# Performance work log

Hardware: AMD Instinct MI355X
Metric: run time of the kernel (lower is better)

Reference implementation:

```python
import jax, jax.numpy as jnp
import numpy as np

N_NODES = 50000
N_EDGES = 800000
IN_DIM = 256
EMB_DIM = 128


def setup_inputs() -> dict:
    key = jax.random.key(0)
    ks = jax.random.split(key, 12)
    x = jax.random.normal(ks[0], (N_NODES, IN_DIM), dtype=jnp.float32)
    edge_index = jax.random.randint(ks[1], (2, N_EDGES), 0, N_NODES, dtype=jnp.int32)
    # Layer 1 params (GCNConv in=256 out=128 with bias, LayerNorm gamma/beta)
    W1 = jax.random.normal(ks[2], (IN_DIM, EMB_DIM), dtype=jnp.float32) / np.sqrt(IN_DIM)
    b1 = jnp.zeros((EMB_DIM,), jnp.float32)
    g1 = jnp.ones((EMB_DIM,), jnp.float32)
    be1 = jnp.zeros((EMB_DIM,), jnp.float32)
    # Layer 2 params (GCNConv in=128 out=128, LayerNorm)
    W2 = jax.random.normal(ks[3], (EMB_DIM, EMB_DIM), dtype=jnp.float32) / np.sqrt(EMB_DIM)
    b2 = jnp.zeros((EMB_DIM,), jnp.float32)
    g2 = jnp.ones((EMB_DIM,), jnp.float32)
    be2 = jnp.zeros((EMB_DIM,), jnp.float32)
    return {"x": x, "W1": W1, "b1": b1, "g1": g1, "be1": be1,
            "W2": W2, "b2": b2, "g2": g2, "be2": be2,
            "edge_index": edge_index}


def _gcn_conv(x, W, b, src, dst, n_nodes):
    # PyG GCNConv: h = x @ W; add self-loops; sym-normalize; scatter-add to dst; + bias
    h = x @ W                                   # [N, out]
    loop = jnp.arange(n_nodes, dtype=src.dtype)
    src_f = jnp.concatenate([src, loop])        # [E+N]
    dst_f = jnp.concatenate([dst, loop])
    deg = jax.ops.segment_sum(jnp.ones_like(dst_f, dtype=h.dtype), dst_f,
                              num_segments=n_nodes)
    dinv = jnp.where(deg > 0, jax.lax.rsqrt(deg), 0.0)
    norm = dinv[src_f] * dinv[dst_f]            # [E+N]
    msg = h[src_f] * norm[:, None]              # gather + scale (memory-bound)
    out = jax.ops.segment_sum(msg, dst_f, num_segments=n_nodes)
    return out + b


def _layer_norm(x, gamma, beta, eps=1e-5):
    mu = jnp.mean(x, axis=-1, keepdims=True)
    var = jnp.mean(jnp.square(x - mu), axis=-1, keepdims=True)
    return (x - mu) * jax.lax.rsqrt(var + eps) * gamma + beta


def reference(x, W1, b1, g1, be1, W2, b2, g2, be2, edge_index):
    src, dst = edge_index[0], edge_index[1]
    n = x.shape[0]
    # Layer 1: in_dim (256) != embed_dim (128) -> no residual
    h = _gcn_conv(x, W1, b1, src, dst, n)
    h = jax.nn.elu(_layer_norm(h, g1, be1))      # dropout = identity (eval mode)
    # Layer 2: dims match -> residual
    res = h
    h2 = _gcn_conv(h, W2, b2, src, dst, n)
    h2 = jax.nn.elu(_layer_norm(h2, g2, be2))
    return h2 + res
```

## Files before the change

kernel.cpp:

```cpp
#include <hip/hip_runtime.h>
#include <hip/hip_bf16.h>

#define NN 50000
#define NE 800000
#define KDIM 256
#define EMB 128
#define NB 391
#define CAP 2560
#define HB 196
#define CWB 192
#define NG1 196
#define NG2 391

typedef unsigned short u16;
typedef __attribute__((ext_vector_type(8))) short short8;
typedef __attribute__((ext_vector_type(4))) float f32x4;

static __device__ __forceinline__ u16 f2bf(float f) {
    union { float f; unsigned int u; } x; x.f = f;
    unsigned int u = x.u;
    unsigned int r = (u + 0x7fffu + ((u >> 16) & 1u)) >> 16;
    return (u16)r;
}
static __device__ __forceinline__ float bf2f(u16 b) {
    union { unsigned int u; float f; } x; x.u = ((unsigned int)b) << 16;
    return x.f;
}
static __device__ __forceinline__ unsigned cvtpk(float lo, float hi) {
    unsigned r;
    asm volatile("v_cvt_pk_bf16_f32 %0, %1, %2" : "=v"(r) : "v"(lo), "v"(hi));
    return r;
}

__global__ __launch_bounds__(256) void prep_kernel(const float* __restrict__ W1,
                                                   const float* __restrict__ W2,
                                                   u16* __restrict__ Wt1,
                                                   u16* __restrict__ Wt2,
                                                   int* __restrict__ bcnt) {
    if (blockIdx.x == CWB) {
        int t = threadIdx.x;
        if (t < NB) bcnt[t] = 0;
        if (t + 256 < NB) bcnt[t + 256] = 0;
        return;
    }
    int i = blockIdx.x * 256 + threadIdx.x;
    if (i < 128 * 256) {
        int n = i >> 8, k = i & 255;
        Wt1[i] = f2bf(W1[k * 128 + n]);
    } else {
        int j = i - 128 * 256;
        if (j < 128 * 128) {
            int n = j >> 7, k = j & 127;
            Wt2[j] = f2bf(W2[k * 128 + n]);
        }
    }
}

template <int K, bool A_BF16, bool FUSE_PA>
__global__ __launch_bounds__(512) void gemm_kernel(
    const void* __restrict__ Av, const u16* __restrict__ Bt, u16* __restrict__ C, int M,
    const int* __restrict__ esrc, const int* __restrict__ edst,
    int* __restrict__ bcnt, unsigned int* __restrict__ packed, int E) {
    __shared__ u16 Bs[128 * K];

    if constexpr (FUSE_PA) {
        if (blockIdx.x < HB) {
            int* hist = (int*)Bs;
            int* base = hist + NB;
            int t = threadIdx.x;
            int i0 = blockIdx.x * 4096;
            int i1 = i0 + 4096 < E ? i0 + 4096 : E;
            for (int b = t; b < NB; b += 512) hist[b] = 0;
            __syncthreads();
            for (int i = i0 + t; i < i1; i += 512) atomicAdd(&hist[edst[i] >> 7], 1);
            __syncthreads();
            for (int b = t; b < NB; b += 512) {
                int c = hist[b];
                base[b] = c ? atomicAdd(&bcnt[b], c) : 0;
                hist[b] = 0;
            }
            __syncthreads();
            for (int i = i0 + t; i < i1; i += 512) {
                int d = edst[i];
                int b = d >> 7;
                int off = base[b] + atomicAdd(&hist[b], 1);
                if (off < CAP)
                    packed[b * CAP + off] = ((unsigned int)esrc[i] << 7) | (unsigned int)(d & 127);
            }
            return;
        }
    }

    int gb = FUSE_PA ? (blockIdx.x - HB) : blockIdx.x;
    int ngb = FUSE_PA ? (gridDim.x - HB) : gridDim.x;
    int tid = threadIdx.x;
    int wave = tid >> 6, lane = tid & 63;
    constexpr int NKS = K / 32;
    constexpr int NCH = 128 * K / 8;
#pragma unroll
    for (int i = 0; i < NCH / 512; i++) {
        int idx = tid + i * 512;
        int n = idx / (K / 8), c = idx % (K / 8);
        int k0 = c * 8;
        uint4 v = *(const uint4*)(Bt + (size_t)n * K + k0);
        *(uint4*)&Bs[(((n >> 4) * NKS + (k0 >> 5)) << 9) + ((n & 15) << 5) + (k0 & 31)] = v;
    }
    __syncthreads();

    int arow = lane & 15;
    int kb = (lane >> 4) * 8;
    int nfrag = (M + 15) / 16;
    for (int frag = gb * 8 + wave; frag < nfrag; frag += ngb * 8) {
        int row0 = frag * 16;
        short8 af[NKS];
        int r = row0 + arow;
        if (r > M - 1) r = M - 1;
        if constexpr (!A_BF16) {
            const float* ap = (const float*)Av + (size_t)r * K + kb;
#pragma unroll
            for (int ks = 0; ks < NKS; ks++) {
                float4 v0 = *(const float4*)(ap + ks * 32);
                float4 v1 = *(const float4*)(ap + ks * 32 + 4);
                uint4 u;
                u.x = cvtpk(v0.x, v0.y);
                u.y = cvtpk(v0.z, v0.w);
                u.z = cvtpk(v1.x, v1.y);
                u.w = cvtpk(v1.z, v1.w);
                af[ks] = *(short8*)&u;
            }
        } else {
            const u16* ap = (const u16*)Av + (size_t)r * K + kb;
#pragma unroll
            for (int ks = 0; ks < NKS; ks++) {
                uint4 u = *(const uint4*)(ap + ks * 32);
                af[ks] = *(short8*)&u;
            }
        }
        f32x4 acc[8];
#pragma unroll
        for (int nf = 0; nf < 8; nf++) acc[nf] = (f32x4){0.f, 0.f, 0.f, 0.f};
#pragma unroll
        for (int ks = 0; ks < NKS; ks++) {
#pragma unroll
            for (int nf = 0; nf < 8; nf++) {
                short8 b = *(const short8*)&Bs[((nf * NKS + ks) << 9) + (arow << 5) + kb];
                acc[nf] = __builtin_amdgcn_mfma_f32_16x16x32_bf16(af[ks], b, acc[nf], 0, 0, 0);
            }
        }
        int rb = row0 + (lane >> 4) * 4;
        int col = lane & 15;
#pragma unroll
        for (int nf = 0; nf < 8; nf++)
#pragma unroll
            for (int rr = 0; rr < 4; rr++) {
                int grow = rb + rr;
                if (grow < M) C[(size_t)grow * 128 + nf * 16 + col] = f2bf(acc[nf][rr]);
            }
    }
}

__global__ __launch_bounds__(256) void passB_kernel(const unsigned int* __restrict__ packed,
                                                    const int* __restrict__ bcnt,
                                                    u16* __restrict__ srcs,
                                                    unsigned int* __restrict__ rowinfo,
                                                    float* __restrict__ dinv, int n) {
    __shared__ int lc[128];
    __shared__ int cur[128];
    int b = blockIdx.x, t = threadIdx.x;
    int nb0 = b << 7;
    int nnodes = (n - nb0) < 128 ? (n - nb0) : 128;
    int cnt = bcnt[b];
    if (cnt > CAP) cnt = CAP;
    int e0 = b * CAP;
    int e1 = e0 + cnt;
    if (t < 128) lc[t] = 0;
    __syncthreads();
    for (int i = e0 + t; i < e1; i += 256) atomicAdd(&lc[packed[i] & 127], 1);
    __syncthreads();
    int myc = (t < 128) ? lc[t] : 0;
    for (int off = 1; off < 128; off <<= 1) {
        int a = (t < 128 && t >= off) ? lc[t - off] : 0;
        __syncthreads();
        if (t < 128) lc[t] += a;
        __syncthreads();
    }
    if (t < 128) {
        int excl = e0 + lc[t] - myc;
        cur[t] = excl;
        if (t < nnodes) {
            rowinfo[nb0 + t] = ((unsigned int)excl << 12) | (unsigned int)myc;
            dinv[nb0 + t] = rsqrtf((float)(myc + 1));
        }
    }
    __syncthreads();
    for (int i = e0 + t; i < e1; i += 256) {
        unsigned int v = packed[i];
        int p = atomicAdd(&cur[v & 127], 1);
        srcs[p] = (u16)(v >> 7);
    }
}

template <bool HAS_RES, bool OUT_BF16>
__global__ __launch_bounds__(256) void agg_kernel(
    const u16* __restrict__ h, const unsigned int* __restrict__ rowinfo,
    const u16* __restrict__ srcs, const float* __restrict__ dinv,
    const float* __restrict__ bias, const float* __restrict__ gamma,
    const float* __restrict__ beta, const u16* __restrict__ resid,
    void* __restrict__ outv, int n) {
    int wave = threadIdx.x >> 6, lane = threadIdx.x & 63;
    int node = blockIdx.x * 4 + wave;
    if (node >= n) return;
    unsigned int ri = rowinfo[node];
    int e0 = ri >> 12;
    int e1 = e0 + (ri & 4095);
    float di = dinv[node];
    int half = lane >> 5, sl = lane & 31;
    float a0 = 0.f, a1 = 0.f, a2 = 0.f, a3 = 0.f;
    for (int base = e0; base < e1; base += 64) {
        int nE = e1 - base;
        if (nE > 64) nE = 64;
        int s = (lane < nE) ? (int)srcs[base + lane] : 0;
        float w = ((lane < nE) ? dinv[s] : 0.f) * di;
        for (int jp = 0; jp < nE; jp += 4) {
            int i0 = jp + half;
            int i1 = jp + 2 + half;
            int ss0 = __shfl(s, i0); float w0 = __shfl(w, i0);
            int ss1 = __shfl(s, i1); float w1 = __shfl(w, i1);
            uint2 v0 = *(const uint2*)(h + (size_t)ss0 * 128 + sl * 4);
            uint2 v1 = *(const uint2*)(h + (size_t)ss1 * 128 + sl * 4);
            a0 += bf2f((u16)v0.x) * w0 + bf2f((u16)v1.x) * w1;
            a1 += bf2f((u16)(v0.x >> 16)) * w0 + bf2f((u16)(v1.x >> 16)) * w1;
            a2 += bf2f((u16)v0.y) * w0 + bf2f((u16)v1.y) * w1;
            a3 += bf2f((u16)(v0.y >> 16)) * w0 + bf2f((u16)(v1.y >> 16)) * w1;
        }
    }
    {
        uint2 v = *(const uint2*)(h + (size_t)node * 128 + sl * 4);
        float sw = (half == 0) ? di * di : 0.f;
        a0 += bf2f((u16)v.x) * sw;
        a1 += bf2f((u16)(v.x >> 16)) * sw;
        a2 += bf2f((u16)v.y) * sw;
        a3 += bf2f((u16)(v.y >> 16)) * sw;
    }
    a0 += __shfl_xor(a0, 32);
    a1 += __shfl_xor(a1, 32);
    a2 += __shfl_xor(a2, 32);
    a3 += __shfl_xor(a3, 32);
    a0 += bias[sl * 4];
    a1 += bias[sl * 4 + 1];
    a2 += bias[sl * 4 + 2];
    a3 += bias[sl * 4 + 3];
    float sum = a0 + a1 + a2 + a3;
    float sq = a0 * a0 + a1 * a1 + a2 * a2 + a3 * a3;
    for (int off = 16; off >= 1; off >>= 1) {
        sum += __shfl_xor(sum, off);
        sq += __shfl_xor(sq, off);
    }
    float mu = sum * (1.f / 128.f);
    float var = sq * (1.f / 128.f) - mu * mu;
    float rs = rsqrtf(var + 1e-5f);
    float o0 = (a0 - mu) * rs * gamma[sl * 4] + beta[sl * 4];
    float o1 = (a1 - mu) * rs * gamma[sl * 4 + 1] + beta[sl * 4 + 1];
    float o2 = (a2 - mu) * rs * gamma[sl * 4 + 2] + beta[sl * 4 + 2];
    float o3 = (a3 - mu) * rs * gamma[sl * 4 + 3] + beta[sl * 4 + 3];
    o0 = o0 > 0.f ? o0 : __expf(o0) - 1.f;
    o1 = o1 > 0.f ? o1 : __expf(o1) - 1.f;
    o2 = o2 > 0.f ? o2 : __expf(o2) - 1.f;
    o3 = o3 > 0.f ? o3 : __expf(o3) - 1.f;
    if constexpr (HAS_RES) {
        uint2 rv = *(const uint2*)(resid + (size_t)node * 128 + sl * 4);
        o0 += bf2f((u16)rv.x);
        o1 += bf2f((u16)(rv.x >> 16));
        o2 += bf2f((u16)rv.y);
        o3 += bf2f((u16)(rv.y >> 16));
    }
    if (half == 0) {
        if constexpr (OUT_BF16) {
            u16* out = (u16*)outv;
            uint2 pk;
            pk.x = (unsigned)f2bf(o0) | ((unsigned)f2bf(o1) << 16);
            pk.y = (unsigned)f2bf(o2) | ((unsigned)f2bf(o3) << 16);
            *(uint2*)(out + (size_t)node * 128 + sl * 4) = pk;
        } else {
            float* out = (float*)outv;
            *(float4*)(out + (size_t)node * 128 + sl * 4) = make_float4(o0, o1, o2, o3);
        }
    }
}

extern "C" void kernel_launch(void* const* d_in, const int* in_sizes, int n_in,
                              void* d_out, int out_size, void* d_ws, size_t ws_size,
                              hipStream_t stream) {
    const float* x   = (const float*)d_in[0];
    const float* W1  = (const float*)d_in[1];
    const float* b1  = (const float*)d_in[2];
    const float* g1  = (const float*)d_in[3];
    const float* be1 = (const float*)d_in[4];
    const float* W2  = (const float*)d_in[5];
    const float* b2  = (const float*)d_in[6];
    const float* g2  = (const float*)d_in[7];
    const float* be2 = (const float*)d_in[8];
    const int* ei    = (const int*)d_in[9];
    const int* srcp  = ei;
    const int* dstp  = ei + NE;
    float* out = (float*)d_out;

    char* ws = (char*)d_ws;
    size_t off = 0;
    auto alloc = [&](size_t bytes) {
        void* p = ws + off;
        off += (bytes + 255) & ~(size_t)255;
        return p;
    };
    int* bcnt        = (int*)alloc(NB * 4);
    unsigned* rowinfo= (unsigned*)alloc(NN * 4);
    float* dinv      = (float*)alloc(NN * 4);
    unsigned* packed = (unsigned*)alloc((size_t)NB * CAP * 4);
    u16* srcs_s      = (u16*)alloc((size_t)NB * CAP * 2);
    u16* Wt1         = (u16*)alloc(128 * 256 * 2);
    u16* Wt2         = (u16*)alloc(128 * 128 * 2);
    u16* hb          = (u16*)alloc((size_t)NN * 128 * 2);
    u16* h1b         = (u16*)alloc((size_t)NN * 128 * 2);

    prep_kernel<<<CWB + 1, 256, 0, stream>>>(W1, W2, Wt1, Wt2, bcnt);
    gemm_kernel<256, false, true><<<HB + NG1, 512, 0, stream>>>(x, Wt1, hb, NN,
                                                                srcp, dstp, bcnt, packed, NE);
    passB_kernel<<<NB, 256, 0, stream>>>(packed, bcnt, srcs_s, rowinfo, dinv, NN);
    agg_kernel<false, true><<<(NN + 3) / 4, 256, 0, stream>>>(hb, rowinfo, srcs_s, dinv,
                                                              b1, g1, be1, nullptr, h1b, NN);
    gemm_kernel<128, true, false><<<NG2, 512, 0, stream>>>(h1b, Wt2, hb, NN,
                                                           nullptr, nullptr, nullptr, nullptr, 0);
    agg_kernel<true, false><<<(NN + 3) / 4, 256, 0, stream>>>(hb, rowinfo, srcs_s, dinv,
                                                              b2, g2, be2, h1b, out, NN);
}
```

Baseline: 129.8 us.

## Split aggregation into feature-sliced gather and separate LayerNorm pass with permuted layout

Splits each aggregation into two kernels. The first gathers neighbour rows one 16-feature slice at a time, with eight blocks per 128-node bucket each owning one slice, so the gathered slice of h is reused from cache. The second applies bias, LayerNorm, ELU and the residual. The GEMM epilogue now writes packed 16-byte stores in a permuted column order. Parameters, W2 rows and the final fp32 output are remapped to match that order. This adds an extra bf16 round-trip through a new hagg buffer, a rounding step before LayerNorm, and scattered fp32 output stores.

```diff
diff --git a/kernel.cpp b/kernel.cpp
--- a/kernel.cpp
+++ b/kernel.cpp
@@ -13,6 +13,7 @@
 #define NG2 391
 
 typedef unsigned short u16;
+typedef unsigned char u8;
 typedef __attribute__((ext_vector_type(8))) short short8;
 typedef __attribute__((ext_vector_type(4))) float f32x4;
 
@@ -31,16 +32,27 @@
     asm volatile("v_cvt_pk_bf16_f32 %0, %1, %2" : "=v"(r) : "v"(lo), "v"(hi));
     return r;
 }
-
-__global__ __launch_bounds__(256) void prep_kernel(const float* __restrict__ W1,
-                                                   const float* __restrict__ W2,
-                                                   u16* __restrict__ Wt1,
-                                                   u16* __restrict__ Wt2,
-                                                   int* __restrict__ bcnt) {
+static __device__ __forceinline__ int p2dim(int p) { return ((p & 7) << 4) + (p >> 3); }
+
+__global__ __launch_bounds__(256) void prep_kernel(
+    const float* __restrict__ W1, const float* __restrict__ W2,
+    u16* __restrict__ Wt1, u16* __restrict__ Wt2, int* __restrict__ bcnt,
+    const float* __restrict__ b1, const float* __restrict__ g1, const float* __restrict__ be1,
+    const float* __restrict__ b2, const float* __restrict__ g2, const float* __restrict__ be2,
+    float* __restrict__ prm) {
     if (blockIdx.x == CWB) {
         int t = threadIdx.x;
         if (t < NB) bcnt[t] = 0;
         if (t + 256 < NB) bcnt[t + 256] = 0;
+        if (t < 128) {
+            int d = p2dim(t);
+            prm[t]       = b1[d];
+            prm[128 + t] = g1[d];
+            prm[256 + t] = be1[d];
+            prm[384 + t] = b2[d];
+            prm[512 + t] = g2[d];
+            prm[640 + t] = be2[d];
+        }
         return;
     }
     int i = blockIdx.x * 256 + threadIdx.x;
@@ -50,15 +62,16 @@
     } else {
         int j = i - 128 * 256;
         if (j < 128 * 128) {
-            int n = j >> 7, k = j & 127;
-            Wt2[j] = f2bf(W2[k * 128 + n]);
+            int n = j >> 7, p = j & 127;
+            Wt2[j] = f2bf(W2[p2dim(p) * 128 + n]);
         }
     }
 }
 
 template <int K, bool A_BF16, bool FUSE_PA>
 __global__ __launch_bounds__(512) void gemm_kernel(
-    const void* __restrict__ Av, const u16* __restrict__ Bt, u16* __restrict__ C, int M,
+    const void* __restrict__ Av, const u16* __restrict__ Bt,
+    u16* __restrict__ Cb, int M,
     const int* __restrict__ esrc, const int* __restrict__ edst,
     int* __restrict__ bcnt, unsigned int* __restrict__ packed, int E) {
     __shared__ u16 Bs[128 * K];
@@ -150,12 +163,17 @@
         int rb = row0 + (lane >> 4) * 4;
         int col = lane & 15;
 #pragma unroll
-        for (int nf = 0; nf < 8; nf++)
-#pragma unroll
-            for (int rr = 0; rr < 4; rr++) {
-                int grow = rb + rr;
-                if (grow < M) C[(size_t)grow * 128 + nf * 16 + col] = f2bf(acc[nf][rr]);
-            }
+        for (int rr = 0; rr < 4; rr++) {
+            int grow = rb + rr;
+            if (grow < M) {
+                uint4 pb;
+                pb.x = cvtpk(acc[0][rr], acc[1][rr]);
+                pb.y = cvtpk(acc[2][rr], acc[3][rr]);
+                pb.z = cvtpk(acc[4][rr], acc[5][rr]);
+                pb.w = cvtpk(acc[6][rr], acc[7][rr]);
+                *(uint4*)(Cb + (size_t)grow * 128 + col * 8) = pb;
+            }
+        }
     }
 }
 
@@ -200,91 +218,84 @@
     }
 }
 
-template <bool HAS_RES, bool OUT_BF16>
-__global__ __launch_bounds__(256) void agg_kernel(
+__global__ __launch_bounds__(256) void aggA_kernel(
     const u16* __restrict__ h, const unsigned int* __restrict__ rowinfo,
     const u16* __restrict__ srcs, const float* __restrict__ dinv,
-    const float* __restrict__ bias, const float* __restrict__ gamma,
-    const float* __restrict__ beta, const u16* __restrict__ resid,
-    void* __restrict__ outv, int n) {
+    u16* __restrict__ hagg, int n) {
+    int dg = blockIdx.x & 7;
+    int bucket = blockIdx.x >> 3;
+    int wave = threadIdx.x >> 6, lane = threadIdx.x & 63;
+    int slot = lane >> 3, j = lane & 7;
+    int doff = dg * 16 + j * 2;
+    int n0 = bucket * 128 + wave * 32;
+    for (int ni = 0; ni < 32; ni++) {
+        int node = n0 + ni;
+        if (node >= n) break;
+        unsigned ri = rowinfo[node];
+        int e0 = ri >> 12;
+        int cnt = ri & 4095;
+        float di = dinv[node];
+        float a0 = 0.f, a1 = 0.f;
+        for (int jp = 0; jp < cnt; jp += 8) {
+            int idx = jp + slot;
+            int valid = idx < cnt;
+            int s = valid ? (int)srcs[e0 + idx] : 0;
+            float w = valid ? dinv[s] * di : 0.f;
+            unsigned v = *(const unsigned*)(h + (size_t)s * 128 + doff);
+            a0 += bf2f((u16)v) * w;
+            a1 += bf2f((u16)(v >> 16)) * w;
+        }
+        {
+            unsigned v = *(const unsigned*)(h + (size_t)node * 128 + doff);
+            float sw = (slot == 0) ? di * di : 0.f;
+            a0 += bf2f((u16)v) * sw;
+            a1 += bf2f((u16)(v >> 16)) * sw;
+        }
+        a0 += __shfl_xor(a0, 8);  a1 += __shfl_xor(a1, 8);
+        a0 += __shfl_xor(a0, 16); a1 += __shfl_xor(a1, 16);
+        a0 += __shfl_xor(a0, 32); a1 += __shfl_xor(a1, 32);
+        if (slot == 0)
+            *(unsigned*)(hagg + (size_t)node * 128 + doff) = cvtpk(a0, a1);
+    }
+}
+
+template <bool HAS_RES, bool OUT_BF16>
+__global__ __launch_bounds__(256) void aggB_kernel(
+    const u16* __restrict__ hagg, const float* __restrict__ prm, int prmoff,
+    const u16* __restrict__ resid, void* __restrict__ outv, int n) {
     int wave = threadIdx.x >> 6, lane = threadIdx.x & 63;
     int node = blockIdx.x * 4 + wave;
     if (node >= n) return;
-    unsigned int ri = rowinfo[node];
-    int e0 = ri >> 12;
-    int e1 = e0 + (ri & 4095);
-    float di = dinv[node];
-    int half = lane >> 5, sl = lane & 31;
-    float a0 = 0.f, a1 = 0.f, a2 = 0.f, a3 = 0.f;
-    for (int base = e0; base < e1; base += 64) {
-        int nE = e1 - base;
-        if (nE > 64) nE = 64;
-        int s = (lane < nE) ? (int)srcs[base + lane] : 0;
-        float w = ((lane < nE) ? dinv[s] : 0.f) * di;
-        for (int jp = 0; jp < nE; jp += 4) {
-            int i0 = jp + half;
-            int i1 = jp + 2 + half;
-            int ss0 = __shfl(s, i0); float w0 = __shfl(w, i0);
-            int ss1 = __shfl(s, i1); float w1 = __shfl(w, i1);
-            uint2 v0 = *(const uint2*)(h + (size_t)ss0 * 128 + sl * 4);
-            uint2 v1 = *(const uint2*)(h + (size_t)ss1 * 128 + sl * 4);
-            a0 += bf2f((u16)v0.x) * w0 + bf2f((u16)v1.x) * w1;
-            a1 += bf2f((u16)(v0.x >> 16)) * w0 + bf2f((u16)(v1.x >> 16)) * w1;
-            a2 += bf2f((u16)v0.y) * w0 + bf2f((u16)v1.y) * w1;
-            a3 += bf2f((u16)(v0.y >> 16)) * w0 + bf2f((u16)(v1.y >> 16)) * w1;
-        }
-    }
-    {
-        uint2 v = *(const uint2*)(h + (size_t)node * 128 + sl * 4);
-        float sw = (half == 0) ? di * di : 0.f;
-        a0 += bf2f((u16)v.x) * sw;
-        a1 += bf2f((u16)(v.x >> 16)) * sw;
-        a2 += bf2f((u16)v.y) * sw;
-        a3 += bf2f((u16)(v.y >> 16)) * sw;
-    }
-    a0 += __shfl_xor(a0, 32);
-    a1 += __shfl_xor(a1, 32);
-    a2 += __shfl_xor(a2, 32);
-    a3 += __shfl_xor(a3, 32);
-    a0 += bias[sl * 4];
-    a1 += bias[sl * 4 + 1];
-    a2 += bias[sl * 4 + 2];
-    a3 += bias[sl * 4 + 3];
-    float sum = a0 + a1 + a2 + a3;
-    float sq = a0 * a0 + a1 * a1 + a2 * a2 + a3 * a3;
-    for (int off = 16; off >= 1; off >>= 1) {
+    const float* bias = prm + prmoff;
+    const float* gamma = bias + 128;
+    const float* beta = gamma + 128;
+    unsigned v = *(const unsigned*)(hagg + (size_t)node * 128 + lane * 2);
+    float a0 = bf2f((u16)v) + bias[lane * 2];
+    float a1 = bf2f((u16)(v >> 16)) + bias[lane * 2 + 1];
+    float sum = a0 + a1, sq = a0 * a0 + a1 * a1;
+    for (int off = 32; off >= 1; off >>= 1) {
         sum += __shfl_xor(sum, off);
         sq += __shfl_xor(sq, off);
     }
     float mu = sum * (1.f / 128.f);
     float var = sq * (1.f / 128.f) - mu * mu;
     float rs = rsqrtf(var + 1e-5f);
-    float o0 = (a0 - mu) * rs * gamma[sl * 4] + beta[sl * 4];
-    float o1 = (a1 - mu) * rs * gamma[sl * 4 + 1] + beta[sl * 4 + 1];
-    float o2 = (a2 - mu) * rs * gamma[sl * 4 + 2] + beta[sl * 4 + 2];
-    float o3 = (a3 - mu) * rs * gamma[sl * 4 + 3] + beta[sl * 4 + 3];
+    float o0 = (a0 - mu) * rs * gamma[lane * 2] + beta[lane * 2];
+    float o1 = (a1 - mu) * rs * gamma[lane * 2 + 1] + beta[lane * 2 + 1];
     o0 = o0 > 0.f ? o0 : __expf(o0) - 1.f;
     o1 = o1 > 0.f ? o1 : __expf(o1) - 1.f;
-    o2 = o2 > 0.f ? o2 : __expf(o2) - 1.f;
-    o3 = o3 > 0.f ? o3 : __expf(o3) - 1.f;
     if constexpr (HAS_RES) {
-        uint2 rv = *(const uint2*)(resid + (size_t)node * 128 + sl * 4);
-        o0 += bf2f((u16)rv.x);
-        o1 += bf2f((u16)(rv.x >> 16));
-        o2 += bf2f((u16)rv.y);
-        o3 += bf2f((u16)(rv.y >> 16));
-    }
-    if (half == 0) {
-        if constexpr (OUT_BF16) {
-            u16* out = (u16*)outv;
-            uint2 pk;
-            pk.x = (unsigned)f2bf(o0) | ((unsigned)f2bf(o1) << 16);
-            pk.y = (unsigned)f2bf(o2) | ((unsigned)f2bf(o3) << 16);
-            *(uint2*)(out + (size_t)node * 128 + sl * 4) = pk;
-        } else {
-            float* out = (float*)outv;
-            *(float4*)(out + (size_t)node * 128 + sl * 4) = make_float4(o0, o1, o2, o3);
-        }
+        unsigned rv = *(const unsigned*)(resid + (size_t)node * 128 + lane * 2);
+        o0 += bf2f((u16)rv);
+        o1 += bf2f((u16)(rv >> 16));
+    }
+    if constexpr (OUT_BF16) {
+        *(unsigned*)((u16*)outv + (size_t)node * 128 + lane * 2) = cvtpk(o0, o1);
+    } else {
+        float* out = (float*)outv + (size_t)node * 128;
+        int p = lane * 2;
+        out[p2dim(p)] = o0;
+        out[p2dim(p + 1)] = o1;
     }
 }
 
@@ -315,21 +326,24 @@
     int* bcnt        = (int*)alloc(NB * 4);
     unsigned* rowinfo= (unsigned*)alloc(NN * 4);
     float* dinv      = (float*)alloc(NN * 4);
+    float* prm       = (float*)alloc(6 * 128 * 4);
     unsigned* packed = (unsigned*)alloc((size_t)NB * CAP * 4);
     u16* srcs_s      = (u16*)alloc((size_t)NB * CAP * 2);
     u16* Wt1         = (u16*)alloc(128 * 256 * 2);
     u16* Wt2         = (u16*)alloc(128 * 128 * 2);
     u16* hb          = (u16*)alloc((size_t)NN * 128 * 2);
+    u16* hagg        = (u16*)alloc((size_t)NN * 128 * 2);
     u16* h1b         = (u16*)alloc((size_t)NN * 128 * 2);
 
-    prep_kernel<<<CWB + 1, 256, 0, stream>>>(W1, W2, Wt1, Wt2, bcnt);
+    prep_kernel<<<CWB + 1, 256, 0, stream>>>(W1, W2, Wt1, Wt2, bcnt,
+                                             b1, g1, be1, b2, g2, be2, prm);
     gemm_kernel<256, false, true><<<HB + NG1, 512, 0, stream>>>(x, Wt1, hb, NN,
                                                                 srcp, dstp, bcnt, packed, NE);
     passB_kernel<<<NB, 256, 0, stream>>>(packed, bcnt, srcs_s, rowinfo, dinv, NN);
-    agg_kernel<false, true><<<(NN + 3) / 4, 256, 0, stream>>>(hb, rowinfo, srcs_s, dinv,
-                                                              b1, g1, be1, nullptr, h1b, NN);
+    aggA_kernel<<<NB * 8, 256, 0, stream>>>(hb, rowinfo, srcs_s, dinv, hagg, NN);
+    aggB_kernel<false, true><<<(NN + 3) / 4, 256, 0, stream>>>(hagg, prm, 0, nullptr, h1b, NN);
     gemm_kernel<128, true, false><<<NG2, 512, 0, stream>>>(h1b, Wt2, hb, NN,
                                                            nullptr, nullptr, nullptr, nullptr, 0);
-    agg_kernel<true, false><<<(NN + 3) / 4, 256, 0, stream>>>(hb, rowinfo, srcs_s, dinv,
-                                                              b2, g2, be2, h1b, out, NN);
-}
+    aggA_kernel<<<NB * 8, 256, 0, stream>>>(hb, rowinfo, srcs_s, dinv, hagg, NN);
+    aggB_kernel<true, false><<<(NN + 3) / 4, 256, 0, stream>>>(hagg, prm, 384, h1b, out, NN);
+}
```

Measured after the change: 456.4 us. +251.5%, slower.

## Store GEMM output in permuted column order with packed 16-byte row writes

Applied to the files above, without the earlier changes.

The GEMM epilogue now packs the eight accumulator fragments per row into one 16-byte bf16 store, replacing scattered 2-byte stores. The hidden dimension is therefore kept in a permuted order. W2 rows, bias, gamma and beta are pre-permuted to match, and the final fp32 output is un-permuted with scalar stores. The layer-1 GEMM grid size also changes. The cost is scattered 4-byte final output writes in place of float4 stores.

```diff
diff --git a/kernel.cpp b/kernel.cpp
--- a/kernel.cpp
+++ b/kernel.cpp
@@ -9,10 +9,11 @@
 #define CAP 2560
 #define HB 196
 #define CWB 192
-#define NG1 196
+#define NG1 316
 #define NG2 391
 
 typedef unsigned short u16;
+typedef unsigned char u8;
 typedef __attribute__((ext_vector_type(8))) short short8;
 typedef __attribute__((ext_vector_type(4))) float f32x4;
 
@@ -31,16 +32,27 @@
     asm volatile("v_cvt_pk_bf16_f32 %0, %1, %2" : "=v"(r) : "v"(lo), "v"(hi));
     return r;
 }
-
-__global__ __launch_bounds__(256) void prep_kernel(const float* __restrict__ W1,
-                                                   const float* __restrict__ W2,
-                                                   u16* __restrict__ Wt1,
-                                                   u16* __restrict__ Wt2,
-                                                   int* __restrict__ bcnt) {
+static __device__ __forceinline__ int p2dim(int p) { return ((p & 7) << 4) + (p >> 3); }
+
+__global__ __launch_bounds__(256) void prep_kernel(
+    const float* __restrict__ W1, const float* __restrict__ W2,
+    u16* __restrict__ Wt1, u16* __restrict__ Wt2, int* __restrict__ bcnt,
+    const float* __restrict__ b1, const float* __restrict__ g1, const float* __restrict__ be1,
+    const float* __restrict__ b2, const float* __restrict__ g2, const float* __restrict__ be2,
+    float* __restrict__ prm) {
     if (blockIdx.x == CWB) {
         int t = threadIdx.x;
         if (t < NB) bcnt[t] = 0;
         if (t + 256 < NB) bcnt[t + 256] = 0;
+        if (t < 128) {
+            int d = p2dim(t);
+            prm[t]       = b1[d];
+            prm[128 + t] = g1[d];
+            prm[256 + t] = be1[d];
+            prm[384 + t] = b2[d];
+            prm[512 + t] = g2[d];
+            prm[640 + t] = be2[d];
+        }
         return;
     }
     int i = blockIdx.x * 256 + threadIdx.x;
@@ -50,15 +62,16 @@
     } else {
         int j = i - 128 * 256;
         if (j < 128 * 128) {
-            int n = j >> 7, k = j & 127;
-            Wt2[j] = f2bf(W2[k * 128 + n]);
+            int n = j >> 7, p = j & 127;
+            Wt2[j] = f2bf(W2[p2dim(p) * 128 + n]);
         }
     }
 }
 
 template <int K, bool A_BF16, bool FUSE_PA>
 __global__ __launch_bounds__(512) void gemm_kernel(
-    const void* __restrict__ Av, const u16* __restrict__ Bt, u16* __restrict__ C, int M,
+    const void* __restrict__ Av, const u16* __restrict__ Bt,
+    u16* __restrict__ Cb, int M,
     const int* __restrict__ esrc, const int* __restrict__ edst,
     int* __restrict__ bcnt, unsigned int* __restrict__ packed, int E) {
     __shared__ u16 Bs[128 * K];
@@ -150,12 +163,17 @@
         int rb = row0 + (lane >> 4) * 4;
         int col = lane & 15;
 #pragma unroll
-        for (int nf = 0; nf < 8; nf++)
-#pragma unroll
-            for (int rr = 0; rr < 4; rr++) {
-                int grow = rb + rr;
-                if (grow < M) C[(size_t)grow * 128 + nf * 16 + col] = f2bf(acc[nf][rr]);
-            }
+        for (int rr = 0; rr < 4; rr++) {
+            int grow = rb + rr;
+            if (grow < M) {
+                uint4 pb;
+                pb.x = cvtpk(acc[0][rr], acc[1][rr]);
+                pb.y = cvtpk(acc[2][rr], acc[3][rr]);
+                pb.z = cvtpk(acc[4][rr], acc[5][rr]);
+                pb.w = cvtpk(acc[6][rr], acc[7][rr]);
+                *(uint4*)(Cb + (size_t)grow * 128 + col * 8) = pb;
+            }
+        }
     }
 }
 
@@ -204,8 +222,7 @@
 __global__ __launch_bounds__(256) void agg_kernel(
     const u16* __restrict__ h, const unsigned int* __restrict__ rowinfo,
     const u16* __restrict__ srcs, const float* __restrict__ dinv,
-    const float* __restrict__ bias, const float* __restrict__ gamma,
-    const float* __restrict__ beta, const u16* __restrict__ resid,
+    const float* __restrict__ prm, int prmoff, const u16* __restrict__ resid,
     void* __restrict__ outv, int n) {
     int wave = threadIdx.x >> 6, lane = threadIdx.x & 63;
     int node = blockIdx.x * 4 + wave;
@@ -246,6 +263,9 @@
     a1 += __shfl_xor(a1, 32);
     a2 += __shfl_xor(a2, 32);
     a3 += __shfl_xor(a3, 32);
+    const float* bias = prm + prmoff;
+    const float* gamma = bias + 128;
+    const float* beta = gamma + 128;
     a0 += bias[sl * 4];
     a1 += bias[sl * 4 + 1];
     a2 += bias[sl * 4 + 2];
@@ -278,12 +298,16 @@
         if constexpr (OUT_BF16) {
             u16* out = (u16*)outv;
             uint2 pk;
-            pk.x = (unsigned)f2bf(o0) | ((unsigned)f2bf(o1) << 16);
-            pk.y = (unsigned)f2bf(o2) | ((unsigned)f2bf(o3) << 16);
+            pk.x = cvtpk(o0, o1);
+            pk.y = cvtpk(o2, o3);
             *(uint2*)(out + (size_t)node * 128 + sl * 4) = pk;
         } else {
-            float* out = (float*)outv;
-            *(float4*)(out + (size_t)node * 128 + sl * 4) = make_float4(o0, o1, o2, o3);
+            float* out = (float*)outv + (size_t)node * 128;
+            int p = sl * 4;
+            out[p2dim(p)]     = o0;
+            out[p2dim(p + 1)] = o1;
+            out[p2dim(p + 2)] = o2;
+            out[p2dim(p + 3)] = o3;
         }
     }
 }
@@ -315,6 +339,7 @@
     int* bcnt        = (int*)alloc(NB * 4);
     unsigned* rowinfo= (unsigned*)alloc(NN * 4);
     float* dinv      = (float*)alloc(NN * 4);
+    float* prm       = (float*)alloc(6 * 128 * 4);
     unsigned* packed = (unsigned*)alloc((size_t)NB * CAP * 4);
     u16* srcs_s      = (u16*)alloc((size_t)NB * CAP * 2);
     u16* Wt1         = (u16*)alloc(128 * 256 * 2);
@@ -322,14 +347,15 @@
     u16* hb          = (u16*)alloc((size_t)NN * 128 * 2);
     u16* h1b         = (u16*)alloc((size_t)NN * 128 * 2);
 
-    prep_kernel<<<CWB + 1, 256, 0, stream>>>(W1, W2, Wt1, Wt2, bcnt);
+    prep_kernel<<<CWB + 1, 256, 0, stream>>>(W1, W2, Wt1, Wt2, bcnt,
+                                             b1, g1, be1, b2, g2, be2, prm);
     gemm_kernel<256, false, true><<<HB + NG1, 512, 0, stream>>>(x, Wt1, hb, NN,
                                                                 srcp, dstp, bcnt, packed, NE);
     passB_kernel<<<NB, 256, 0, stream>>>(packed, bcnt, srcs_s, rowinfo, dinv, NN);
     agg_kernel<false, true><<<(NN + 3) / 4, 256, 0, stream>>>(hb, rowinfo, srcs_s, dinv,
-                                                              b1, g1, be1, nullptr, h1b, NN);
+                                                              prm, 0, nullptr, h1b, NN);
     gemm_kernel<128, true, false><<<NG2, 512, 0, stream>>>(h1b, Wt2, hb, NN,
                                                            nullptr, nullptr, nullptr, nullptr, 0);
     agg_kernel<true, false><<<(NN + 3) / 4, 256, 0, stream>>>(hb, rowinfo, srcs_s, dinv,
-                                                              b2, g2, be2, h1b, out, NN);
-}
+                                                              prm, 384, h1b, out, NN);
+}
```

Result: no change. 127.3 us (-1.9%).
